# Performance work log

Measured on AMD Instinct MI355X. Metric: run time of the kernel, lower is better.

The kernel has to match this reference:

```python
import jax, jax.numpy as jnp
import numpy as np

BETA = 0.25
EPS_NORM = 1e-12

def _l2norm(x):
    # F.normalize(x, dim=-1): x / max(||x||, eps)
    n = jnp.sqrt(jnp.sum(x * x, axis=-1, keepdims=True))
    return x / jnp.maximum(n, EPS_NORM)

def setup_inputs() -> dict:
    key = jax.random.key(0)
    k1, k2 = jax.random.split(key)
    z = jax.random.normal(k1, (32, 4096, 256), dtype=jnp.float32)
    # matches nn.Embedding init uniform_(-1/num_embed, 1/num_embed)
    embed_weight = jax.random.uniform(k2, (1024, 256), dtype=jnp.float32,
                                      minval=-1.0 / 1024, maxval=1.0 / 1024)
    return {"z": z, "embed_weight": embed_weight}

def reference(z, embed_weight):
    num_embed, embed_dim = embed_weight.shape
    z_flat = z.reshape(-1, embed_dim)                      # [N, D]
    n_tok = z_flat.shape[0]

    # cosine distance: normalized z (detached) @ normalized codebook^T -> [N, K]
    zn = jax.lax.stop_gradient(_l2norm(z_flat))
    cn = _l2norm(embed_weight)
    d = zn @ cn.T                                          # [N, K]

    # torch sort(dim=1) then indices[:, -1] == argmax along codebook axis
    encoding_indices = jnp.argmax(d, axis=1)               # [N] int

    z_q = embed_weight[encoding_indices].reshape(z.shape)  # gather codebook rows

    # training losses (commitment + codebook)
    sg = jax.lax.stop_gradient
    loss = BETA * jnp.mean((sg(z_q) - z) ** 2) + jnp.mean((z_q - sg(z)) ** 2)

    # straight-through estimator
    z_q_st = z + sg(z_q - z)

    # perplexity from one-hot usage stats (counts instead of dense one-hot)
    counts = jnp.zeros((num_embed,), jnp.float32).at[encoding_indices].add(1.0)
    avg_probs = counts / jnp.float32(n_tok)
    perplexity = jnp.exp(-jnp.sum(avg_probs * jnp.log(avg_probs + 1e-10)))

    return z_q_st, loss, perplexity, encoding_indices
```

## Files before the change

kernel.cpp:

```cpp
#include <hip/hip_runtime.h>
#include <math.h>

#define N_TOK   131072
#define DIM     256
#define K_CODE  1024
#define KEXT    768
#define MARGIN  2e-3f

#define WS_COUNTS   0
#define WS_LOSS     4096
#define WS_RCOUNT   4104
#define WS_INVN     8192
#define WS_FIDX     16384
#define WS_RLIST    1048576
#define WS_BEXT     2097152

#define CHUNK_BYTES 49152

#define OUT_LOSS  33554432
#define OUT_PERP  33554433
#define OUT_IDX   33554434

typedef __bf16 bf16x8 __attribute__((ext_vector_type(8)));
typedef float  f32x4  __attribute__((ext_vector_type(4)));

static __device__ __forceinline__ unsigned short f2bf(float f) {
    unsigned int u = __float_as_uint(f);
    u += 0x7FFFu + ((u >> 16) & 1u);
    return (unsigned short)(u >> 16);
}
static __device__ __forceinline__ float bf2f(unsigned short h) {
    return __uint_as_float(((unsigned int)h) << 16);
}

static __device__ __forceinline__ void load_lds16(const void* g, void* l) {
    __builtin_amdgcn_global_load_lds(
        (const __attribute__((address_space(1))) unsigned int*)g,
        (__attribute__((address_space(3))) unsigned int*)l, 16, 0, 0);
}

__global__ void vq_norms(const float* __restrict__ embed, float* __restrict__ invn) {
    int lane = threadIdx.x & 63;
    int wave = (blockIdx.x * blockDim.x + threadIdx.x) >> 6;
    int nwav = (gridDim.x * blockDim.x) >> 6;
    for (int k = wave; k < K_CODE; k += nwav) {
        float4 v = *(const float4*)&embed[k * DIM + lane * 4];
        float s = v.x * v.x + v.y * v.y + v.z * v.z + v.w * v.w;
        #pragma unroll
        for (int off = 32; off; off >>= 1) s += __shfl_xor(s, off);
        if (lane == 0) invn[k] = 1.0f / fmaxf(sqrtf(s), 1e-12f);
    }
}

__global__ void vq_pack(const float* __restrict__ embed, unsigned short* __restrict__ bext) {
    int id = blockIdx.x * 256 + threadIdx.x;
    int k   = id / 96;
    int j8  = id - k * 96;
    int kk0 = j8 * 8;
    int src, hi;
    if (kk0 < 256)      { src = kk0;       hi = 1; }
    else if (kk0 < 512) { src = kk0 - 256; hi = 0; }
    else                { src = kk0 - 512; hi = 1; }
    const float* e = &embed[k * DIM + src];
    float4 f0 = *(const float4*)e;
    float4 f1 = *(const float4*)(e + 4);
    float v[8] = {f0.x, f0.y, f0.z, f0.w, f1.x, f1.y, f1.z, f1.w};
    unsigned short r[8] __attribute__((aligned(16)));
    #pragma unroll
    for (int j = 0; j < 8; ++j) {
        unsigned short h = f2bf(v[j]);
        r[j] = hi ? h : f2bf(v[j] - bf2f(h));
    }
    int c = k >> 5, kin = k & 31;
    int nt = kin >> 4, col = kin & 15;
    int ks = kk0 >> 5, quad = (kk0 >> 3) & 3;
    size_t dst = (size_t)c * CHUNK_BYTES + (size_t)(((nt * 24 + ks) * 64) + quad * 16 + col) * 16;
    *(float4*)((char*)bext + dst) = *(const float4*)r;
}

__launch_bounds__(512, 2)
__global__ void vq_argmax(const float* __restrict__ z,
                          const unsigned short* __restrict__ bext,
                          const float* __restrict__ invn, int* __restrict__ fidx,
                          int* __restrict__ rcount, int* __restrict__ rlist) {
    __shared__ unsigned short b0[CHUNK_BYTES / 2];
    __shared__ unsigned short b1[CHUNK_BYTES / 2];
    __shared__ float invn_s[K_CODE];

    const int tid  = threadIdx.x;
    const int w    = tid >> 6;
    const int lane = tid & 63;
    const int col  = lane & 15;
    const int quad = lane >> 4;
    const int tokBase = blockIdx.x * 256;

    invn_s[tid]       = invn[tid];
    invn_s[tid + 512] = invn[tid + 512];
    asm volatile("s_waitcnt lgkmcnt(0)" ::: "memory");

    bf16x8 ah[2][8], al[2][8];
    #pragma unroll
    for (int mt = 0; mt < 2; ++mt) {
        const float* zr = z + (size_t)(tokBase + w * 32 + mt * 16 + col) * DIM;
        #pragma unroll
        for (int ks = 0; ks < 8; ++ks) {
            float4 f0 = *(const float4*)(zr + ks * 32 + quad * 8);
            float4 f1 = *(const float4*)(zr + ks * 32 + quad * 8 + 4);
            float v[8] = {f0.x, f0.y, f0.z, f0.w, f1.x, f1.y, f1.z, f1.w};
            union { bf16x8 v; unsigned short u[8]; } th, tl;
            #pragma unroll
            for (int j = 0; j < 8; ++j) {
                unsigned short h = f2bf(v[j]);
                th.u[j] = h;
                tl.u[j] = f2bf(v[j] - bf2f(h));
            }
            ah[mt][ks] = th.v;
            al[mt][ks] = tl.v;
        }
    }

    auto stage = [&](int c, unsigned short* buf) {
        const char* gsrc = (const char*)bext + (size_t)c * CHUNK_BYTES;
        #pragma unroll
        for (int i = 0; i < 6; ++i) {
            int seg = w * 6 + i;
            load_lds16(gsrc + (size_t)seg * 1024 + lane * 16,
                       (char*)buf + seg * 1024);
        }
    };

    float best[2][4], second[2][4];
    int   bidx[2][4];
    #pragma unroll
    for (int mt = 0; mt < 2; ++mt)
        #pragma unroll
        for (int r = 0; r < 4; ++r) { best[mt][r] = -1e30f; second[mt][r] = -1e30f; bidx[mt][r] = 0; }

    auto compute = [&](int c, const unsigned short* bbuf) {
        f32x4 acc[2][2];
        #pragma unroll
        for (int mt = 0; mt < 2; ++mt)
            #pragma unroll
            for (int nt = 0; nt < 2; ++nt) acc[mt][nt] = (f32x4){0.f, 0.f, 0.f, 0.f};

        __builtin_amdgcn_s_setprio(1);
        #pragma unroll
        for (int nt = 0; nt < 2; ++nt) {
            const unsigned short* bb = bbuf + nt * 24 * 512;
            #pragma unroll
            for (int ks = 0; ks < 8; ++ks) {
                bf16x8 b = *(const bf16x8*)&bb[ks * 512 + lane * 8];
                acc[0][nt] = __builtin_amdgcn_mfma_f32_16x16x32_bf16(ah[0][ks], b, acc[0][nt], 0, 0, 0);
                acc[1][nt] = __builtin_amdgcn_mfma_f32_16x16x32_bf16(ah[1][ks], b, acc[1][nt], 0, 0, 0);
            }
            #pragma unroll
            for (int ks = 0; ks < 8; ++ks) {
                bf16x8 b = *(const bf16x8*)&bb[(8 + ks) * 512 + lane * 8];
                acc[0][nt] = __builtin_amdgcn_mfma_f32_16x16x32_bf16(ah[0][ks], b, acc[0][nt], 0, 0, 0);
                acc[1][nt] = __builtin_amdgcn_mfma_f32_16x16x32_bf16(ah[1][ks], b, acc[1][nt], 0, 0, 0);
            }
            #pragma unroll
            for (int ks = 0; ks < 8; ++ks) {
                bf16x8 b = *(const bf16x8*)&bb[(16 + ks) * 512 + lane * 8];
                acc[0][nt] = __builtin_amdgcn_mfma_f32_16x16x32_bf16(al[0][ks], b, acc[0][nt], 0, 0, 0);
                acc[1][nt] = __builtin_amdgcn_mfma_f32_16x16x32_bf16(al[1][ks], b, acc[1][nt], 0, 0, 0);
            }
        }
        __builtin_amdgcn_s_setprio(0);

        #pragma unroll
        for (int nt = 0; nt < 2; ++nt) {
            int code = c * 32 + nt * 16 + col;
            float iv = invn_s[code];
            #pragma unroll
            for (int mt = 0; mt < 2; ++mt)
                #pragma unroll
                for (int r = 0; r < 4; ++r) {
                    float v = acc[mt][nt][r] * iv;
                    if (v > best[mt][r]) { second[mt][r] = best[mt][r]; best[mt][r] = v; bidx[mt][r] = code; }
                    else                 { second[mt][r] = fmaxf(second[mt][r], v); }
                }
        }
    };

    __builtin_amdgcn_sched_barrier(0);
    stage(0, b0);
    stage(1, b1);

    #pragma unroll 1
    for (int cc = 0; cc < 32; cc += 2) {
        asm volatile("s_waitcnt vmcnt(6)" ::: "memory");
        __builtin_amdgcn_s_barrier();
        __builtin_amdgcn_sched_barrier(0);
        compute(cc, b0);
        __builtin_amdgcn_sched_barrier(0);
        __builtin_amdgcn_s_barrier();
        if (cc + 2 < 32) stage(cc + 2, b0);

        if (cc == 30) { asm volatile("s_waitcnt vmcnt(0)" ::: "memory"); }
        else          { asm volatile("s_waitcnt vmcnt(6)" ::: "memory"); }
        __builtin_amdgcn_s_barrier();
        __builtin_amdgcn_sched_barrier(0);
        compute(cc + 1, b1);
        __builtin_amdgcn_sched_barrier(0);
        __builtin_amdgcn_s_barrier();
        if (cc + 3 < 32) stage(cc + 3, b1);
    }

    #pragma unroll
    for (int mt = 0; mt < 2; ++mt)
        #pragma unroll
        for (int r = 0; r < 4; ++r) {
            float B = best[mt][r], S = second[mt][r];
            int   I = bidx[mt][r];
            #pragma unroll
            for (int off = 1; off < 16; off <<= 1) {
                float ob = __shfl_xor(B, off);
                float os = __shfl_xor(S, off);
                int   oi = __shfl_xor(I, off);
                if (ob > B) {
                    S = fmaxf(B, os);
                    B = ob; I = oi;
                } else {
                    if (ob == B && oi < I) I = oi;
                    S = fmaxf(S, ob);
                }
            }
            if (col == 0) {
                int token = tokBase + w * 32 + mt * 16 + quad * 4 + r;
                fidx[token] = I;
                if (B - S < MARGIN) {
                    int p = atomicAdd(rcount, 1);
                    rlist[p] = token;
                }
            }
        }
}

__global__ void vq_recheck(const float* __restrict__ z, const float* __restrict__ embed,
                           const int* __restrict__ rcount, const int* __restrict__ rlist,
                           int* __restrict__ fidx) {
    __shared__ double zd[DIM];
    __shared__ double rv[256];
    __shared__ int    rix[256];
    const int cnt = *rcount;
    for (int li = blockIdx.x; li < cnt; li += gridDim.x) {
        int token = rlist[li];
        __syncthreads();
        zd[threadIdx.x] = (double)z[token * DIM + threadIdx.x];
        __syncthreads();
        double bv = -1e300;
        int    bi = 0;
        #pragma unroll
        for (int j = 0; j < 4; ++j) {
            int k = threadIdx.x * 4 + j;
            const float* e = &embed[k * DIM];
            double acc = 0.0, nrm = 0.0;
            for (int d = 0; d < DIM; d += 4) {
                float4 ef = *(const float4*)&e[d];
                acc += (double)ef.x * zd[d]     + (double)ef.y * zd[d + 1] +
                       (double)ef.z * zd[d + 2] + (double)ef.w * zd[d + 3];
                nrm += (double)ef.x * ef.x + (double)ef.y * ef.y +
                       (double)ef.z * ef.z + (double)ef.w * ef.w;
            }
            double val = acc / fmax(sqrt(nrm), 1e-12);
            if (val > bv) { bv = val; bi = k; }
        }
        rv[threadIdx.x]  = bv;
        rix[threadIdx.x] = bi;
        __syncthreads();
        for (int s = 128; s; s >>= 1) {
            if (threadIdx.x < s) {
                double v2 = rv[threadIdx.x + s];
                int    i2 = rix[threadIdx.x + s];
                if (v2 > rv[threadIdx.x] ||
                    (v2 == rv[threadIdx.x] && i2 < rix[threadIdx.x])) {
                    rv[threadIdx.x] = v2;
                    rix[threadIdx.x] = i2;
                }
            }
            __syncthreads();
        }
        if (threadIdx.x == 0) fidx[token] = rix[0];
    }
}

__global__ void vq_output(const float* __restrict__ z, const float* __restrict__ embed,
                          const int* __restrict__ fidx, float* __restrict__ out,
                          int* __restrict__ counts, double* __restrict__ lossAcc) {
    int lane = threadIdx.x & 63;
    int gw   = (blockIdx.x * blockDim.x + threadIdx.x) >> 6;
    int nwav = (gridDim.x * blockDim.x) >> 6;
    double lsum = 0.0;
    for (int t = gw; t < N_TOK; t += nwav) {
        int idx = fidx[t];
        float4 e  = *(const float4*)&embed[idx * DIM + lane * 4];
        float4 zz = *(const float4*)&z[(size_t)t * DIM + lane * 4];
        float4 r, o;
        r.x = e.x - zz.x; r.y = e.y - zz.y; r.z = e.z - zz.z; r.w = e.w - zz.w;
        o.x = zz.x + r.x; o.y = zz.y + r.y; o.z = zz.z + r.z; o.w = zz.w + r.w;
        *(float4*)&out[(size_t)t * DIM + lane * 4] = o;
        lsum += (double)r.x * r.x + (double)r.y * r.y +
                (double)r.z * r.z + (double)r.w * r.w;
        if (lane == 0) {
            atomicAdd(&counts[idx], 1);
            out[OUT_IDX + t] = (float)idx;
        }
    }
    #pragma unroll
    for (int off = 32; off; off >>= 1) lsum += __shfl_down(lsum, off);
    if (lane == 0) atomicAdd(lossAcc, lsum);
}

__global__ void vq_finalize(const int* __restrict__ counts,
                            const double* __restrict__ lossAcc,
                            float* __restrict__ out) {
    __shared__ double sh[256];
    double s = 0.0;
    for (int b = threadIdx.x; b < K_CODE; b += 256) {
        double p = (double)counts[b] / (double)N_TOK;
        s += p * log(p + 1e-10);
    }
    sh[threadIdx.x] = s;
    __syncthreads();
    for (int st = 128; st; st >>= 1) {
        if (threadIdx.x < st) sh[threadIdx.x] += sh[threadIdx.x + st];
        __syncthreads();
    }
    if (threadIdx.x == 0) {
        out[OUT_PERP] = (float)exp(-sh[0]);
        out[OUT_LOSS] = (float)(1.25 * (*lossAcc) / (double)(N_TOK) / (double)(DIM));
    }
}

extern "C" void kernel_launch(void* const* d_in, const int* in_sizes, int n_in,
                              void* d_out, int out_size, void* d_ws, size_t ws_size,
                              hipStream_t stream) {
    const float* z     = (const float*)d_in[0];
    const float* embed = (const float*)d_in[1];
    float* out = (float*)d_out;
    char*  ws  = (char*)d_ws;

    int*            counts  = (int*)   (ws + WS_COUNTS);
    double*         lossAcc = (double*)(ws + WS_LOSS);
    int*            rcount  = (int*)   (ws + WS_RCOUNT);
    float*          invn    = (float*) (ws + WS_INVN);
    int*            fidx    = (int*)   (ws + WS_FIDX);
    int*            rlist   = (int*)   (ws + WS_RLIST);
    unsigned short* bext    = (unsigned short*)(ws + WS_BEXT);

    hipMemsetAsync(ws, 0, 16384, stream);

    vq_norms  <<<16,   256, 0, stream>>>(embed, invn);
    vq_pack   <<<384,  256, 0, stream>>>(embed, bext);
    vq_argmax <<<N_TOK / 256, 512, 0, stream>>>(z, bext, invn, fidx, rcount, rlist);
    vq_recheck<<<512,  256, 0, stream>>>(z, embed, rcount, rlist, fidx);
    vq_output <<<2048, 256, 0, stream>>>(z, embed, fidx, out, counts, lossAcc);
    vq_finalize<<<1,   256, 0, stream>>>(counts, lossAcc, out);
}
```

Baseline: 642.4 us.

## Triple-buffer codebook chunks and interleave staged loads with MFMA phases

```diff
diff --git a/kernel.cpp b/kernel.cpp
--- a/kernel.cpp
+++ b/kernel.cpp
@@ -16,6 +16,7 @@
 #define WS_BEXT     2097152
 
 #define CHUNK_BYTES 49152
+#define CHUNK_SH    (CHUNK_BYTES / 2)
 
 #define OUT_LOSS  33554432
 #define OUT_PERP  33554433
@@ -83,8 +84,7 @@
                           const unsigned short* __restrict__ bext,
                           const float* __restrict__ invn, int* __restrict__ fidx,
                           int* __restrict__ rcount, int* __restrict__ rlist) {
-    __shared__ unsigned short b0[CHUNK_BYTES / 2];
-    __shared__ unsigned short b1[CHUNK_BYTES / 2];
+    __shared__ unsigned short btri[3 * CHUNK_SH];
     __shared__ float invn_s[K_CODE];
 
     const int tid  = threadIdx.x;
@@ -119,13 +119,13 @@
         }
     }
 
-    auto stage = [&](int c, unsigned short* buf) {
+    auto stage_pair = [&](int c, int bslot, int pair) {
         const char* gsrc = (const char*)bext + (size_t)c * CHUNK_BYTES;
-        #pragma unroll
-        for (int i = 0; i < 6; ++i) {
-            int seg = w * 6 + i;
-            load_lds16(gsrc + (size_t)seg * 1024 + lane * 16,
-                       (char*)buf + seg * 1024);
+        char* ldst = (char*)(btri + bslot * CHUNK_SH);
+        #pragma unroll
+        for (int i = 0; i < 2; ++i) {
+            int seg = w * 6 + pair * 2 + i;
+            load_lds16(gsrc + (size_t)seg * 1024 + lane * 16, ldst + seg * 1024);
         }
     };
 
@@ -136,76 +136,83 @@
         #pragma unroll
         for (int r = 0; r < 4; ++r) { best[mt][r] = -1e30f; second[mt][r] = -1e30f; bidx[mt][r] = 0; }
 
-    auto compute = [&](int c, const unsigned short* bbuf) {
+    __builtin_amdgcn_sched_barrier(0);
+    #pragma unroll
+    for (int p = 0; p < 3; ++p) stage_pair(0, 0, p);
+    #pragma unroll
+    for (int p = 0; p < 3; ++p) stage_pair(1, 1, p);
+    asm volatile("s_waitcnt vmcnt(6)" ::: "memory");
+    __builtin_amdgcn_sched_barrier(0);
+    __builtin_amdgcn_s_barrier();
+
+#define PHASE(ntv, koff, AF, SC, SSLOT, SP)                                     \
+    {                                                                           \
+        const unsigned short* bb = bufc + (ntv) * 24 * 512;                     \
+        bf16x8 breg[8];                                                         \
+        _Pragma("unroll")                                                       \
+        for (int j = 0; j < 8; ++j)                                             \
+            breg[j] = *(const bf16x8*)&bb[((koff) + j) * 512 + lane * 8];       \
+        if ((SC) < 32) stage_pair((SC), (SSLOT), (SP));                         \
+        __builtin_amdgcn_sched_barrier(0);                                      \
+        __builtin_amdgcn_s_barrier();                                           \
+        asm volatile("s_waitcnt lgkmcnt(0)" ::: "memory");                      \
+        __builtin_amdgcn_sched_barrier(0);                                      \
+        __builtin_amdgcn_s_setprio(1);                                          \
+        _Pragma("unroll")                                                       \
+        for (int j = 0; j < 8; ++j) {                                           \
+            acc[0][ntv] = __builtin_amdgcn_mfma_f32_16x16x32_bf16(AF[0][j], breg[j], acc[0][ntv], 0, 0, 0); \
+            acc[1][ntv] = __builtin_amdgcn_mfma_f32_16x16x32_bf16(AF[1][j], breg[j], acc[1][ntv], 0, 0, 0); \
+        }                                                                       \
+        __builtin_amdgcn_s_setprio(0);                                          \
+        __builtin_amdgcn_sched_barrier(0);                                      \
+    }
+
+#define EPI(ntv)                                                                \
+    {                                                                           \
+        int code = c * 32 + (ntv) * 16 + col;                                   \
+        float iv = invn_s[code];                                                \
+        _Pragma("unroll")                                                       \
+        for (int mt = 0; mt < 2; ++mt)                                          \
+            _Pragma("unroll")                                                   \
+            for (int r = 0; r < 4; ++r) {                                       \
+                float v = acc[mt][ntv][r] * iv;                                 \
+                if (v > best[mt][r]) { second[mt][r] = best[mt][r]; best[mt][r] = v; bidx[mt][r] = code; } \
+                else                 { second[mt][r] = fmaxf(second[mt][r], v); } \
+            }                                                                   \
+    }
+
+    int slot = 0;
+    int pslot = 2;
+    #pragma unroll 1
+    for (int c = 0; c < 32; ++c) {
+        const unsigned short* bufc = btri + slot * CHUNK_SH;
+        const int sc = c + 2;
+
         f32x4 acc[2][2];
         #pragma unroll
         for (int mt = 0; mt < 2; ++mt)
             #pragma unroll
             for (int nt = 0; nt < 2; ++nt) acc[mt][nt] = (f32x4){0.f, 0.f, 0.f, 0.f};
 
-        __builtin_amdgcn_s_setprio(1);
-        #pragma unroll
-        for (int nt = 0; nt < 2; ++nt) {
-            const unsigned short* bb = bbuf + nt * 24 * 512;
-            #pragma unroll
-            for (int ks = 0; ks < 8; ++ks) {
-                bf16x8 b = *(const bf16x8*)&bb[ks * 512 + lane * 8];
-                acc[0][nt] = __builtin_amdgcn_mfma_f32_16x16x32_bf16(ah[0][ks], b, acc[0][nt], 0, 0, 0);
-                acc[1][nt] = __builtin_amdgcn_mfma_f32_16x16x32_bf16(ah[1][ks], b, acc[1][nt], 0, 0, 0);
-            }
-            #pragma unroll
-            for (int ks = 0; ks < 8; ++ks) {
-                bf16x8 b = *(const bf16x8*)&bb[(8 + ks) * 512 + lane * 8];
-                acc[0][nt] = __builtin_amdgcn_mfma_f32_16x16x32_bf16(ah[0][ks], b, acc[0][nt], 0, 0, 0);
-                acc[1][nt] = __builtin_amdgcn_mfma_f32_16x16x32_bf16(ah[1][ks], b, acc[1][nt], 0, 0, 0);
-            }
-            #pragma unroll
-            for (int ks = 0; ks < 8; ++ks) {
-                bf16x8 b = *(const bf16x8*)&bb[(16 + ks) * 512 + lane * 8];
-                acc[0][nt] = __builtin_amdgcn_mfma_f32_16x16x32_bf16(al[0][ks], b, acc[0][nt], 0, 0, 0);
-                acc[1][nt] = __builtin_amdgcn_mfma_f32_16x16x32_bf16(al[1][ks], b, acc[1][nt], 0, 0, 0);
-            }
-        }
-        __builtin_amdgcn_s_setprio(0);
-
-        #pragma unroll
-        for (int nt = 0; nt < 2; ++nt) {
-            int code = c * 32 + nt * 16 + col;
-            float iv = invn_s[code];
-            #pragma unroll
-            for (int mt = 0; mt < 2; ++mt)
-                #pragma unroll
-                for (int r = 0; r < 4; ++r) {
-                    float v = acc[mt][nt][r] * iv;
-                    if (v > best[mt][r]) { second[mt][r] = best[mt][r]; best[mt][r] = v; bidx[mt][r] = code; }
-                    else                 { second[mt][r] = fmaxf(second[mt][r], v); }
-                }
-        }
-    };
-
-    __builtin_amdgcn_sched_barrier(0);
-    stage(0, b0);
-    stage(1, b1);
-
-    #pragma unroll 1
-    for (int cc = 0; cc < 32; cc += 2) {
-        asm volatile("s_waitcnt vmcnt(6)" ::: "memory");
-        __builtin_amdgcn_s_barrier();
-        __builtin_amdgcn_sched_barrier(0);
-        compute(cc, b0);
+        PHASE(0, 0,  ah, sc, pslot, 0);  __builtin_amdgcn_s_barrier();
+        PHASE(0, 8,  ah, sc, pslot, 1);  __builtin_amdgcn_s_barrier();
+        PHASE(0, 16, al, sc, pslot, 2);  EPI(0);
         __builtin_amdgcn_sched_barrier(0);
         __builtin_amdgcn_s_barrier();
-        if (cc + 2 < 32) stage(cc + 2, b0);
-
-        if (cc == 30) { asm volatile("s_waitcnt vmcnt(0)" ::: "memory"); }
-        else          { asm volatile("s_waitcnt vmcnt(6)" ::: "memory"); }
-        __builtin_amdgcn_s_barrier();
+        PHASE(1, 0,  ah, 32, 0, 0);      __builtin_amdgcn_s_barrier();
+        PHASE(1, 8,  ah, 32, 0, 0);      __builtin_amdgcn_s_barrier();
+        PHASE(1, 16, al, 32, 0, 0);      EPI(1);
         __builtin_amdgcn_sched_barrier(0);
-        compute(cc + 1, b1);
+        if (c == 30)      { asm volatile("s_waitcnt vmcnt(0)" ::: "memory"); }
+        else if (c < 30)  { asm volatile("s_waitcnt vmcnt(6)" ::: "memory"); }
         __builtin_amdgcn_sched_barrier(0);
         __builtin_amdgcn_s_barrier();
-        if (cc + 3 < 32) stage(cc + 3, b1);
-    }
+
+        slot  = (slot  == 2) ? 0 : slot + 1;
+        pslot = (pslot == 2) ? 0 : pslot + 1;
+    }
+#undef PHASE
+#undef EPI
 
     #pragma unroll
     for (int mt = 0; mt < 2; ++mt)
```

Measured after the change: 653.4 us. No clear change (+1.7%).
